# Optimization experiments

Hardware: AMD Instinct MI355X
Metric: run time of the kernel (lower is better)

## Reference

```python
import jax, jax.numpy as jnp
import numpy as np

ALPHA = 0.2  # LeakyReLU negative slope


def _gat_layer(x, W, a):
    """One GraphAttentionLayer (concat=True -> elu output).
    x: (B,N,Din); W: (Din,F); a: (2F,1).
    Faithful to source: adj mask is computed then discarded (softmax over raw e),
    so adj does not enter the math. Uses the additive decomposition
    e_ij = leakyrelu(a1.h_i + a2.h_j) which is mathematically identical to the
    dense (N,N,2F) concat in the original.
    """
    h = x @ W                      # (B,N,F)
    F = W.shape[1]
    a1, a2 = a[:F, 0], a[F:, 0]    # (F,), (F,)
    f1 = h @ a1                    # (B,N)
    f2 = h @ a2                    # (B,N)
    e = jax.nn.leaky_relu(f1[:, :, None] + f2[:, None, :], negative_slope=ALPHA)  # (B,N,N)
    att = jax.nn.softmax(e, axis=-1)
    h_prime = jnp.einsum('bnm,bmf->bnf', att, h)
    return jax.nn.elu(h_prime)


def setup_inputs() -> dict:
    key = jax.random.key(0)
    ks = jax.random.split(key, 6)
    B, N, D, H, F = 8, 1024, 256, 8, 128
    x = jax.random.normal(ks[0], (B, N, D), jnp.float32)
    adj = (jax.random.uniform(ks[1], (N, N)) > 0.9).astype(jnp.float32)
    xavier = lambda fi, fo: 1.414 * (2.0 / (fi + fo)) ** 0.5
    W_heads = jax.random.normal(ks[2], (H, D, F), jnp.float32) * xavier(D, F)
    a_heads = jax.random.normal(ks[3], (H, 2 * F, 1), jnp.float32) * xavier(2 * F, 1)
    W_out = jax.random.normal(ks[4], (H * F, F), jnp.float32) * xavier(H * F, F)
    a_out = jax.random.normal(ks[5], (2 * F, 1), jnp.float32) * xavier(2 * F, 1)
    return {"x": x, "adj": adj, "W_heads": W_heads, "a_heads": a_heads,
            "W_out": W_out, "a_out": a_out}


def reference(x, adj, W_heads, a_heads, W_out, a_out):
    # GAT.forward (dropout omitted: eval mode identity). adj unused per source bug.
    heads = jax.vmap(lambda W, a: _gat_layer(x, W, a))(W_heads, a_heads)  # (H,B,N,F)
    B, N = x.shape[0], x.shape[1]
    xc = jnp.transpose(heads, (1, 2, 0, 3)).reshape(B, N, -1)  # concat heads: (B,N,H*F)
    # out_att has concat=True (applies elu), then GAT.forward applies elu again.
    return jax.nn.elu(_gat_layer(xc, W_out, a_out))
```

## Files before the change

kernel.cpp:

```cpp
#include <hip/hip_runtime.h>
#include <math.h>

#define ALPHA 0.2f
#define LOG2E 1.44269504089f

typedef __attribute__((ext_vector_type(8))) short bf16x8;
typedef __attribute__((ext_vector_type(4))) float f32x4;

__device__ __forceinline__ float elu1(float x)  { return x > 0.f ? x : (__expf(x) - 1.f); }

__device__ __forceinline__ unsigned short f2bf(float x) {
    unsigned u = __float_as_uint(x);
    return (unsigned short)((u + 0x7fffu + ((u >> 16) & 1u)) >> 16);
}
__device__ __forceinline__ unsigned pkbf16(float a, float b) {
    return (unsigned)f2bf(a) | ((unsigned)f2bf(b) << 16);
}
__device__ __forceinline__ float bfs(unsigned short v) { return __uint_as_float((unsigned)v << 16); }
__device__ __forceinline__ unsigned pkbf_rhu(float a, float b) {
    unsigned ua = __float_as_uint(a) + 0x8000u;
    unsigned ub = __float_as_uint(b) + 0x8000u;
    return __builtin_amdgcn_perm(ub, ua, 0x07060302u);
}

__global__ __launch_bounds__(256) void cvt_w_all(
    const float* __restrict__ Wh, const float* __restrict__ Wo,
    unsigned short* __restrict__ WhT, unsigned short* __restrict__ WoT)
{
    const int z = blockIdx.z;
    const int K = (z < 8) ? 256 : 1024;
    if (blockIdx.x * 64 >= K) return;
    const float* in = (z < 8) ? (Wh + (size_t)z * K * 128) : Wo;
    unsigned short* out = (z < 8) ? (WhT + (size_t)z * 128 * K) : WoT;

    __shared__ float T[64][65];
    const int tid = threadIdx.x;
    const int k0 = blockIdx.x * 64, n0 = blockIdx.y * 64;

    const int kr = tid >> 4, nc = (tid & 15) * 4;
#pragma unroll
    for (int s = 0; s < 4; ++s) {
        float4 v = *(const float4*)(in + (size_t)(k0 + kr + s * 16) * 128 + n0 + nc);
        T[kr + s * 16][nc]     = v.x;
        T[kr + s * 16][nc + 1] = v.y;
        T[kr + s * 16][nc + 2] = v.z;
        T[kr + s * 16][nc + 3] = v.w;
    }
    __syncthreads();
    const int nr0 = tid >> 3, kc = (tid & 7) * 8;
#pragma unroll
    for (int s = 0; s < 2; ++s) {
        int nr = nr0 + s * 32;
        unsigned pk[4];
#pragma unroll
        for (int q = 0; q < 4; ++q)
            pk[q] = pkbf16(T[kc + 2 * q][nr], T[kc + 2 * q + 1][nr]);
        *(uint4*)(out + (size_t)(n0 + nr) * K + k0 + kc) = make_uint4(pk[0], pk[1], pk[2], pk[3]);
    }
}

template <int BM, int BN, int WM, int WN, int DOF, int AF32, int THREADS>
__global__ __launch_bounds__(THREADS) void gemm_t(
    const void* __restrict__ Avp, const unsigned short* __restrict__ Bt,
    unsigned short* __restrict__ Ct, int K,
    const float* __restrict__ aV, float* __restrict__ f1g, float* __restrict__ f2g)
{
    const int RM = WM / 16, RN = WN / 16;
    const int NCA = BM * 8 / THREADS, NCB = BN * 8 / THREADS;
    constexpr int SAB_A = (BM + BN) * 72;
    constexpr int SAB_B = BN * (BM + 8) + THREADS * 4;
    constexpr int SAB_SH = SAB_A > SAB_B ? SAB_A : SAB_B;
    __shared__ __align__(16) unsigned short SAB[SAB_SH];
    unsigned short (*As)[72] = (unsigned short(*)[72])SAB;
    unsigned short (*Bs)[72] = (unsigned short(*)[72])(SAB + BM * 72);
    unsigned short (*Cs)[BM + 8] = (unsigned short(*)[BM + 8])SAB;
    float* redf = (float*)(SAB + BN * (BM + 8));

    const int tid = threadIdx.x;
    const int w = tid >> 6, lane = tid & 63;
    const int n16 = lane & 15, quad = lane >> 4;
    const int WX = BM / WM;
    const int wm = (w % WX) * WM, wn = (w / WX) * WN;
    const int m0 = blockIdx.x * BM, n0 = blockIdx.y * BN;

    const float* Af = (const float*)Avp;
    const unsigned short* Ab = (const unsigned short*)Avp;
    const int ar = tid >> 2, akc = (tid & 3) * 16;

    f32x4 acc[RM][RN];
#pragma unroll
    for (int mm = 0; mm < RM; ++mm)
#pragma unroll
        for (int nn = 0; nn < RN; ++nn) acc[mm][nn] = (f32x4){0.f, 0.f, 0.f, 0.f};

    uint4 ra[NCA ? NCA : 1], rb[NCB];
    float4 raf[4];
    if (AF32) {
#pragma unroll
        for (int j = 0; j < 4; ++j)
            raf[j] = *(const float4*)(Af + (size_t)(m0 + ar) * K + akc + 4 * j);
    } else {
#pragma unroll
        for (int i = 0; i < NCA; ++i) {
            int c = tid * NCA + i, r = c >> 3, cc = (c & 7) * 8;
            ra[i] = *(const uint4*)(Ab + (size_t)(m0 + r) * K + cc);
        }
    }
#pragma unroll
    for (int i = 0; i < NCB; ++i) {
        int c = tid * NCB + i, r = c >> 3, cc = (c & 7) * 8;
        rb[i] = *(const uint4*)(Bt + (size_t)(n0 + r) * K + cc);
    }

    const int nk = K >> 6;
    for (int kt = 0; kt < nk; ++kt) {
        __syncthreads();
        if (AF32) {
            uint4 lo = make_uint4(pkbf16(raf[0].x, raf[0].y), pkbf16(raf[0].z, raf[0].w),
                                  pkbf16(raf[1].x, raf[1].y), pkbf16(raf[1].z, raf[1].w));
            uint4 hi = make_uint4(pkbf16(raf[2].x, raf[2].y), pkbf16(raf[2].z, raf[2].w),
                                  pkbf16(raf[3].x, raf[3].y), pkbf16(raf[3].z, raf[3].w));
            *(uint4*)&As[ar][akc]     = lo;
            *(uint4*)&As[ar][akc + 8] = hi;
        } else {
#pragma unroll
            for (int i = 0; i < NCA; ++i) {
                int c = tid * NCA + i, r = c >> 3, cc = (c & 7) * 8;
                *(uint4*)&As[r][cc] = ra[i];
            }
        }
#pragma unroll
        for (int i = 0; i < NCB; ++i) {
            int c = tid * NCB + i, r = c >> 3, cc = (c & 7) * 8;
            *(uint4*)&Bs[r][cc] = rb[i];
        }
        __syncthreads();
        if (kt + 1 < nk) {
            int k0 = (kt + 1) * 64;
            if (AF32) {
#pragma unroll
                for (int j = 0; j < 4; ++j)
                    raf[j] = *(const float4*)(Af + (size_t)(m0 + ar) * K + k0 + akc + 4 * j);
            } else {
#pragma unroll
                for (int i = 0; i < NCA; ++i) {
                    int c = tid * NCA + i, r = c >> 3, cc = (c & 7) * 8;
                    ra[i] = *(const uint4*)(Ab + (size_t)(m0 + r) * K + k0 + cc);
                }
            }
#pragma unroll
            for (int i = 0; i < NCB; ++i) {
                int c = tid * NCB + i, r = c >> 3, cc = (c & 7) * 8;
                rb[i] = *(const uint4*)(Bt + (size_t)(n0 + r) * K + k0 + cc);
            }
        }
#pragma unroll
        for (int ks = 0; ks < 2; ++ks) {
            bf16x8 am[RM], bn[RN];
#pragma unroll
            for (int mm = 0; mm < RM; ++mm)
                am[mm] = *(const bf16x8*)&As[wm + mm * 16 + n16][ks * 32 + quad * 8];
#pragma unroll
            for (int nn = 0; nn < RN; ++nn)
                bn[nn] = *(const bf16x8*)&Bs[wn + nn * 16 + n16][ks * 32 + quad * 8];
#pragma unroll
            for (int mm = 0; mm < RM; ++mm)
#pragma unroll
                for (int nn = 0; nn < RN; ++nn)
                    acc[mm][nn] = __builtin_amdgcn_mfma_f32_16x16x32_bf16(
                        am[mm], bn[nn], acc[mm][nn], 0, 0, 0);
        }
    }

    __syncthreads();

#pragma unroll
    for (int nn = 0; nn < RN; ++nn) {
        int n = wn + nn * 16 + n16;
#pragma unroll
        for (int mm = 0; mm < RM; ++mm) {
            int m = wm + mm * 16 + quad * 4;
            f32x4 a = acc[mm][nn];
            ushort4 o = make_ushort4(f2bf(a[0]), f2bf(a[1]), f2bf(a[2]), f2bf(a[3]));
            *(ushort4*)&Cs[n][m] = o;
        }
    }
    __syncthreads();

    const int CHUNKS = BM * 2 / 16;
    const int RPP = THREADS / CHUNKS;
    const int row = tid / CHUNKS, ch = tid % CHUNKS;
#pragma unroll
    for (int s = 0; s < BN / RPP; ++s) {
        int n = row + s * RPP;
        *(uint4*)(Ct + (size_t)(n0 + n) * 8192 + m0 + ch * 8) =
            *(const uint4*)&Cs[n][ch * 8];
    }

    if (DOF) {
        const int G = THREADS / BM;
        const int FP = 128 / G;
        const int mloc = tid % BM, fq = tid / BM;
        const float* az = aV + blockIdx.y * 256;
        float s1 = 0.f, s2 = 0.f;
#pragma unroll 8
        for (int k = 0; k < FP; ++k) {
            int f = fq * FP + k;
            float h = bfs(Cs[f][mloc]);
            s1 += h * az[f];
            s2 += h * az[128 + f];
        }
        *(float2*)&redf[(fq * BM + mloc) * 2] = make_float2(s1, s2);
        __syncthreads();
        if (tid < BM) {
            float a1 = 0.f, a2 = 0.f;
#pragma unroll
            for (int g = 0; g < G; ++g) {
                a1 += redf[(g * BM + tid) * 2];
                a2 += redf[(g * BM + tid) * 2 + 1];
            }
            f1g[(size_t)blockIdx.y * 8192 + m0 + tid] = a1;
            f2g[(size_t)blockIdx.y * 8192 + m0 + tid] = a2;
        }
    }
}

template <int NI, int NT, int THREADS>
__global__ __launch_bounds__(THREADS) void attn4(
    const unsigned short* __restrict__ hT, const float* __restrict__ f1g,
    const float* __restrict__ f2g, unsigned short* __restrict__ outb)
{
    const int N = 1024, JT = 128, JP = JT + 8;
    const int KKN = JT / 32;
    const int NW = THREADS / 64;
    const int ITILE = 16 * NI * NW;
    const int SJW = JT / 8;
    const int SR = THREADS / SJW;
    const int NTS = NT * 16 / SR;
    const int EPT = 1024 / THREADS;
    __shared__ __align__(16) unsigned short hls[2][NT * 16][JP];
    __shared__ float ul[1024], vl[1024];
    __shared__ float wred[NW];

    const int tid = threadIdx.x;
    const int w = tid >> 6, lane = tid & 63;
    const int n16 = lane & 15, quad = lane >> 4;
    const int hy = blockIdx.x;
    const int bz = blockIdx.z;
    const int ibx = blockIdx.y;
    const int hb = hy * 8 + bz;
    const int iw0 = ibx * ITILE + w * (16 * NI);

    if (EPT == 4) {
        const int j4 = tid * 4;
        float4 fv = *(const float4*)(f2g + (size_t)hb * N + j4);
        fv.x *= LOG2E; fv.y *= LOG2E; fv.z *= LOG2E; fv.w *= LOG2E;
        *(float4*)&ul[j4] = fv;
        float m4 = fmaxf(fmaxf(fv.x, fv.y), fmaxf(fv.z, fv.w));
#pragma unroll
        for (int off = 32; off; off >>= 1) m4 = fmaxf(m4, __shfl_xor(m4, off));
        if (lane == 0) wred[w] = m4;
    } else {
        const int j2 = tid * 2;
        float2 fv = *(const float2*)(f2g + (size_t)hb * N + j2);
        fv.x *= LOG2E; fv.y *= LOG2E;
        *(float2*)&ul[j2] = fv;
        float m4 = fmaxf(fv.x, fv.y);
#pragma unroll
        for (int off = 32; off; off >>= 1) m4 = fmaxf(m4, __shfl_xor(m4, off));
        if (lane == 0) wred[w] = m4;
    }

    float f1L[NI];
#pragma unroll
    for (int ii = 0; ii < NI; ++ii)
        f1L[ii] = f1g[(size_t)hb * N + iw0 + ii * 16 + n16] * LOG2E;

    const unsigned short* gsrc = hT + (size_t)(hy * 128) * 8192 + bz * 1024;
    const int sf = tid / SJW, sj = (tid % SJW) * 8;

    bf16x8 stg[NTS];
#pragma unroll
    for (int s = 0; s < NTS; ++s)
        stg[s] = *(const bf16x8*)(gsrc + (size_t)(sf + SR * s) * 8192 + sj);

    __syncthreads();
    float f2mL = wred[0];
#pragma unroll
    for (int k = 1; k < NW; ++k) f2mL = fmaxf(f2mL, wred[k]);

    if (EPT == 4) {
        const int j4 = tid * 4;
        float4 raw = *(const float4*)&ul[j4];
        float4 uu, vv;
        float d0 = raw.x - f2mL, d1 = raw.y - f2mL, d2 = raw.z - f2mL, d3 = raw.w - f2mL;
        uu.x = __builtin_amdgcn_exp2f(d0); vv.x = __builtin_amdgcn_exp2f(ALPHA * d0);
        uu.y = __builtin_amdgcn_exp2f(d1); vv.y = __builtin_amdgcn_exp2f(ALPHA * d1);
        uu.z = __builtin_amdgcn_exp2f(d2); vv.z = __builtin_amdgcn_exp2f(ALPHA * d2);
        uu.w = __builtin_amdgcn_exp2f(d3); vv.w = __builtin_amdgcn_exp2f(ALPHA * d3);
        *(float4*)&ul[j4] = uu;
        *(float4*)&vl[j4] = vv;
    } else {
        const int j2 = tid * 2;
        float2 raw = *(const float2*)&ul[j2];
        float d0 = raw.x - f2mL, d1 = raw.y - f2mL;
        float2 uu, vv;
        uu.x = __builtin_amdgcn_exp2f(d0); vv.x = __builtin_amdgcn_exp2f(ALPHA * d0);
        uu.y = __builtin_amdgcn_exp2f(d1); vv.y = __builtin_amdgcn_exp2f(ALPHA * d1);
        *(float2*)&ul[j2] = uu;
        *(float2*)&vl[j2] = vv;
    }

    float ri[NI];
#pragma unroll
    for (int ii = 0; ii < NI; ++ii)
        ri[ii] = __builtin_amdgcn_exp2f((ALPHA - 1.f) * (f1L[ii] + f2mL));

    f32x4 acc[NI][NT], accl[NI];
#pragma unroll
    for (int ii = 0; ii < NI; ++ii) {
        accl[ii] = (f32x4){0.f, 0.f, 0.f, 0.f};
#pragma unroll
        for (int t = 0; t < NT; ++t) acc[ii][t] = (f32x4){0.f, 0.f, 0.f, 0.f};
    }
    bf16x8 ones;
    { union { bf16x8 v; unsigned u[4]; } o;
      o.u[0] = o.u[1] = o.u[2] = o.u[3] = 0x3F803F80u; ones = o.v; }

#pragma unroll
    for (int s = 0; s < NTS; ++s)
        *(bf16x8*)&hls[0][sf + SR * s][sj] = stg[s];
    __syncthreads();

    for (int jt = 0; jt < N / JT; ++jt) {
        const int cur = jt & 1;
        if (jt + 1 < N / JT) {
            int j0n = (jt + 1) * JT;
#pragma unroll
            for (int s = 0; s < NTS; ++s)
                stg[s] = *(const bf16x8*)(gsrc + (size_t)(sf + SR * s) * 8192 + j0n + sj);
        }
        const int j0 = jt * JT;
#pragma unroll
        for (int kk = 0; kk < KKN; ++kk) {
            const int jb = j0 + kk * 32 + quad * 8;
            float4 u0 = *(const float4*)&ul[jb], u1 = *(const float4*)&ul[jb + 4];
            float4 v0 = *(const float4*)&vl[jb], v1 = *(const float4*)&vl[jb + 4];
            float uj[8] = {u0.x, u0.y, u0.z, u0.w, u1.x, u1.y, u1.z, u1.w};
            float vj[8] = {v0.x, v0.y, v0.z, v0.w, v1.x, v1.y, v1.z, v1.w};

            bf16x8 afr[NI];
#pragma unroll
            for (int ii = 0; ii < NI; ++ii) {
                union { bf16x8 v; unsigned u[4]; } cvt;
#pragma unroll
                for (int q = 0; q < 4; ++q) {
                    float p0 = fmaxf(uj[2 * q],     ri[ii] * vj[2 * q]);
                    float p1 = fmaxf(uj[2 * q + 1], ri[ii] * vj[2 * q + 1]);
                    cvt.u[q] = pkbf_rhu(p0, p1);
                }
                afr[ii] = cvt.v;
            }
#pragma unroll
            for (int t = 0; t < NT; ++t) {
                bf16x8 bfr = *(const bf16x8*)&hls[cur][t * 16 + n16][kk * 32 + quad * 8];
#pragma unroll
                for (int ii = 0; ii < NI; ++ii)
                    acc[ii][t] = __builtin_amdgcn_mfma_f32_16x16x32_bf16(
                        afr[ii], bfr, acc[ii][t], 0, 0, 0);
            }
#pragma unroll
            for (int ii = 0; ii < NI; ++ii)
                accl[ii] = __builtin_amdgcn_mfma_f32_16x16x32_bf16(
                    afr[ii], ones, accl[ii], 0, 0, 0);
        }
        if (jt + 1 < N / JT) {
#pragma unroll
            for (int s = 0; s < NTS; ++s)
                *(bf16x8*)&hls[1 - cur][sf + SR * s][sj] = stg[s];
        }
        __syncthreads();
    }

#pragma unroll
    for (int ii = 0; ii < NI; ++ii) {
#pragma unroll
        for (int r = 0; r < 4; ++r) {
            float inv = 1.f / accl[ii][r];
            int i = iw0 + ii * 16 + quad * 4 + r;
#pragma unroll
            for (int t = 0; t < NT; ++t) {
                float tv = acc[ii][t][r] * inv;
                tv = elu1(tv);
                outb[(size_t)(bz * 1024 + i) * 1024 + hy * 128 + t * 16 + n16] = f2bf(tv);
            }
        }
    }
}

__global__ __launch_bounds__(256) void attn5(
    const unsigned short* __restrict__ hT, const float* __restrict__ f1g,
    const float* __restrict__ f2g, float* __restrict__ outf)
{
    const int N = 1024;
    __shared__ __align__(16) unsigned short hfull[64][1032];
    __shared__ float ul[1024], vl[1024];
    __shared__ float wred[4];

    const int tid = threadIdx.x;
    const int w = tid >> 6, lane = tid & 63;
    const int n16 = lane & 15, quad = lane >> 4;
    const int bz = blockIdx.x;
    const int ibx = blockIdx.y;
    const int fz = blockIdx.z;
    const int iw0 = ibx * 64 + w * 16;

    const int j4 = tid * 4;
    {
        float4 fv = *(const float4*)(f2g + (size_t)bz * N + j4);
        fv.x *= LOG2E; fv.y *= LOG2E; fv.z *= LOG2E; fv.w *= LOG2E;
        *(float4*)&ul[j4] = fv;
        float m4 = fmaxf(fmaxf(fv.x, fv.y), fmaxf(fv.z, fv.w));
#pragma unroll
        for (int off = 32; off; off >>= 1) m4 = fmaxf(m4, __shfl_xor(m4, off));
        if (lane == 0) wred[w] = m4;
    }

    float f1L = f1g[(size_t)bz * N + iw0 + n16] * LOG2E;

    const unsigned short* gsrc = hT + (size_t)(fz * 64) * 8192 + bz * 1024;
    const int sr = tid >> 3;
    const int sc = (tid & 7) * 8;
#pragma unroll
    for (int s = 0; s < 2; ++s)
#pragma unroll
        for (int c = 0; c < 16; ++c)
            *(bf16x8*)&hfull[sr + 32 * s][sc + c * 64] =
                *(const bf16x8*)(gsrc + (size_t)(sr + 32 * s) * 8192 + sc + c * 64);

    __syncthreads();
    const float f2mL = fmaxf(fmaxf(wred[0], wred[1]), fmaxf(wred[2], wred[3]));

    {
        float4 raw = *(const float4*)&ul[j4];
        float4 uu, vv;
        float d0 = raw.x - f2mL, d1 = raw.y - f2mL, d2 = raw.z - f2mL, d3 = raw.w - f2mL;
        uu.x = __builtin_amdgcn_exp2f(d0); vv.x = __builtin_amdgcn_exp2f(ALPHA * d0);
        uu.y = __builtin_amdgcn_exp2f(d1); vv.y = __builtin_amdgcn_exp2f(ALPHA * d1);
        uu.z = __builtin_amdgcn_exp2f(d2); vv.z = __builtin_amdgcn_exp2f(ALPHA * d2);
        uu.w = __builtin_amdgcn_exp2f(d3); vv.w = __builtin_amdgcn_exp2f(ALPHA * d3);
        *(float4*)&ul[j4] = uu;
        *(float4*)&vl[j4] = vv;
    }
    const float ri = __builtin_amdgcn_exp2f((ALPHA - 1.f) * (f1L + f2mL));

    f32x4 acc[4], accl = (f32x4){0.f, 0.f, 0.f, 0.f};
#pragma unroll
    for (int t = 0; t < 4; ++t) acc[t] = (f32x4){0.f, 0.f, 0.f, 0.f};
    bf16x8 ones;
    { union { bf16x8 v; unsigned u[4]; } o;
      o.u[0] = o.u[1] = o.u[2] = o.u[3] = 0x3F803F80u; ones = o.v; }

    __syncthreads();

    for (int jt = 0; jt < 16; ++jt) {
#pragma unroll
        for (int kk = 0; kk < 2; ++kk) {
            const int jb = jt * 64 + kk * 32 + quad * 8;
            float4 u0 = *(const float4*)&ul[jb], u1 = *(const float4*)&ul[jb + 4];
            float4 v0 = *(const float4*)&vl[jb], v1 = *(const float4*)&vl[jb + 4];
            float uj[8] = {u0.x, u0.y, u0.z, u0.w, u1.x, u1.y, u1.z, u1.w};
            float vj[8] = {v0.x, v0.y, v0.z, v0.w, v1.x, v1.y, v1.z, v1.w};

            union { bf16x8 v; unsigned u[4]; } cvt;
#pragma unroll
            for (int q = 0; q < 4; ++q) {
                float p0 = fmaxf(uj[2 * q],     ri * vj[2 * q]);
                float p1 = fmaxf(uj[2 * q + 1], ri * vj[2 * q + 1]);
                cvt.u[q] = pkbf_rhu(p0, p1);
            }
            bf16x8 afr = cvt.v;
#pragma unroll
            for (int t = 0; t < 4; ++t) {
                bf16x8 bfr = *(const bf16x8*)&hfull[t * 16 + n16][jb];
                acc[t] = __builtin_amdgcn_mfma_f32_16x16x32_bf16(afr, bfr, acc[t], 0, 0, 0);
            }
            accl = __builtin_amdgcn_mfma_f32_16x16x32_bf16(afr, ones, accl, 0, 0, 0);
        }
    }

#pragma unroll
    for (int r = 0; r < 4; ++r) {
        float inv = 1.f / accl[r];
        int i = iw0 + quad * 4 + r;
#pragma unroll
        for (int t = 0; t < 4; ++t) {
            float tv = elu1(elu1(acc[t][r] * inv));
            outf[(size_t)(bz * 1024 + i) * 128 + fz * 64 + t * 16 + n16] = tv;
        }
    }
}

extern "C" void kernel_launch(void* const* d_in, const int* in_sizes, int n_in,
                              void* d_out, int out_size, void* d_ws, size_t ws_size,
                              hipStream_t stream)
{
    const float* x  = (const float*)d_in[0];
    const float* Wh = (const float*)d_in[2];
    const float* ah = (const float*)d_in[3];
    const float* Wo = (const float*)d_in[4];
    const float* ao = (const float*)d_in[5];
    float* out = (float*)d_out;

    unsigned short* WhT = (unsigned short*)d_ws;
    unsigned short* WoT = WhT + 262144;
    unsigned short* h1T = WoT + 131072;
    unsigned short* xcb = h1T + 8388608;
    unsigned short* h2T = xcb + 8388608;
    float* f1a  = (float*)(h2T + 1048576);
    float* f2a  = f1a + 65536;
    float* f1b  = f2a + 65536;
    float* f2b  = f1b + 8192;

    cvt_w_all<<<dim3(16, 2, 9), 256, 0, stream>>>(Wh, Wo, WhT, WoT);

    gemm_t<128, 128, 32, 64, 1, 1, 512><<<dim3(64, 8), 512, 0, stream>>>(
        x, WhT, h1T, 256, ah, f1a, f2a);
    attn4<2, 8, 512><<<dim3(8, 4, 8), 512, 0, stream>>>(h1T, f1a, f2a, xcb);

    gemm_t<32, 128, 16, 64, 1, 0, 256><<<dim3(256, 1), 256, 0, stream>>>(
        xcb, WoT, h2T, 1024, ao, f1b, f2b);
    attn5<<<dim3(8, 16, 2), 256, 0, stream>>>(h2T, f1b, f2b, out);
}
```

Before: 153.4 us.

## Fuse layer-2 projection GEMM and attention into one cooperative kernel with grid sync

The second-layer projection GEMM (with its f1/f2 score reductions) and the final attention kernel are merged into a single cooperative kernel of 256 blocks. A grid-wide sync separates the two phases, and both phases reuse one large shared-memory buffer. This removes a kernel launch boundary and its tail gap. In exchange it pays for the grid sync and runs both phases at the same 256-block, single-block-per-CU occupancy, since the large shared allocation likely limits residency.

```diff
diff --git a/kernel.cpp b/kernel.cpp
--- a/kernel.cpp
+++ b/kernel.cpp
@@ -1,5 +1,8 @@
 #include <hip/hip_runtime.h>
+#include <hip/hip_cooperative_groups.h>
 #include <math.h>
+
+namespace cg = cooperative_groups;
 
 #define ALPHA 0.2f
 #define LOG2E 1.44269504089f
@@ -398,105 +401,215 @@
     }
 }
 
-__global__ __launch_bounds__(256) void attn5(
-    const unsigned short* __restrict__ hT, const float* __restrict__ f1g,
-    const float* __restrict__ f2g, float* __restrict__ outf)
+__global__ __launch_bounds__(256) void l2_fused(
+    const unsigned short* __restrict__ Ab, const unsigned short* __restrict__ Bt,
+    unsigned short* __restrict__ Ct, const float* __restrict__ aV,
+    float* __restrict__ f1g, float* __restrict__ f2g, float* __restrict__ outf)
 {
-    const int N = 1024;
-    __shared__ __align__(16) unsigned short hfull[64][1032];
-    __shared__ float ul[1024], vl[1024];
-    __shared__ float wred[4];
-
+    __shared__ __align__(16) unsigned char SMEM[140320];
     const int tid = threadIdx.x;
     const int w = tid >> 6, lane = tid & 63;
     const int n16 = lane & 15, quad = lane >> 4;
-    const int bz = blockIdx.x;
-    const int ibx = blockIdx.y;
-    const int fz = blockIdx.z;
-    const int iw0 = ibx * 64 + w * 16;
-
-    const int j4 = tid * 4;
+
     {
-        float4 fv = *(const float4*)(f2g + (size_t)bz * N + j4);
-        fv.x *= LOG2E; fv.y *= LOG2E; fv.z *= LOG2E; fv.w *= LOG2E;
-        *(float4*)&ul[j4] = fv;
-        float m4 = fmaxf(fmaxf(fv.x, fv.y), fmaxf(fv.z, fv.w));
-#pragma unroll
-        for (int off = 32; off; off >>= 1) m4 = fmaxf(m4, __shfl_xor(m4, off));
-        if (lane == 0) wred[w] = m4;
-    }
-
-    float f1L = f1g[(size_t)bz * N + iw0 + n16] * LOG2E;
-
-    const unsigned short* gsrc = hT + (size_t)(fz * 64) * 8192 + bz * 1024;
-    const int sr = tid >> 3;
-    const int sc = (tid & 7) * 8;
-#pragma unroll
-    for (int s = 0; s < 2; ++s)
-#pragma unroll
-        for (int c = 0; c < 16; ++c)
-            *(bf16x8*)&hfull[sr + 32 * s][sc + c * 64] =
-                *(const bf16x8*)(gsrc + (size_t)(sr + 32 * s) * 8192 + sc + c * 64);
-
-    __syncthreads();
-    const float f2mL = fmaxf(fmaxf(wred[0], wred[1]), fmaxf(wred[2], wred[3]));
+        const int K = 1024;
+        unsigned short* SMs = (unsigned short*)SMEM;
+        unsigned short (*As)[72] = (unsigned short(*)[72])SMs;
+        unsigned short (*Bs)[72] = (unsigned short(*)[72])(SMs + 32 * 72);
+        unsigned short (*Cs)[40] = (unsigned short(*)[40])SMs;
+        float* redf = (float*)(SMs + 128 * 40);
+
+        const int wm = (w & 1) * 16, wn = (w >> 1) * 64;
+        const int m0 = blockIdx.x * 32;
+        const int ar_r = tid >> 3, ar_c = (tid & 7) * 8;
+
+        f32x4 acc[4];
+#pragma unroll
+        for (int nn = 0; nn < 4; ++nn) acc[nn] = (f32x4){0.f, 0.f, 0.f, 0.f};
+
+        uint4 ra, rb[4];
+        ra = *(const uint4*)(Ab + (size_t)(m0 + ar_r) * K + ar_c);
+#pragma unroll
+        for (int i = 0; i < 4; ++i) {
+            int c = tid * 4 + i, r = c >> 3, cc = (c & 7) * 8;
+            rb[i] = *(const uint4*)(Bt + (size_t)r * K + cc);
+        }
+
+        const int nk = K >> 6;
+        for (int kt = 0; kt < nk; ++kt) {
+            __syncthreads();
+            *(uint4*)&As[ar_r][ar_c] = ra;
+#pragma unroll
+            for (int i = 0; i < 4; ++i) {
+                int c = tid * 4 + i, r = c >> 3, cc = (c & 7) * 8;
+                *(uint4*)&Bs[r][cc] = rb[i];
+            }
+            __syncthreads();
+            if (kt + 1 < nk) {
+                int k0 = (kt + 1) * 64;
+                ra = *(const uint4*)(Ab + (size_t)(m0 + ar_r) * K + k0 + ar_c);
+#pragma unroll
+                for (int i = 0; i < 4; ++i) {
+                    int c = tid * 4 + i, r = c >> 3, cc = (c & 7) * 8;
+                    rb[i] = *(const uint4*)(Bt + (size_t)r * K + k0 + cc);
+                }
+            }
+#pragma unroll
+            for (int ks = 0; ks < 2; ++ks) {
+                bf16x8 am = *(const bf16x8*)&As[wm + n16][ks * 32 + quad * 8];
+                bf16x8 bn[4];
+#pragma unroll
+                for (int nn = 0; nn < 4; ++nn)
+                    bn[nn] = *(const bf16x8*)&Bs[wn + nn * 16 + n16][ks * 32 + quad * 8];
+#pragma unroll
+                for (int nn = 0; nn < 4; ++nn)
+                    acc[nn] = __builtin_amdgcn_mfma_f32_16x16x32_bf16(
+                        am, bn[nn], acc[nn], 0, 0, 0);
+            }
+        }
+
+        __syncthreads();
+#pragma unroll
+        for (int nn = 0; nn < 4; ++nn) {
+            int n = wn + nn * 16 + n16;
+            int m = wm + quad * 4;
+            f32x4 a = acc[nn];
+            ushort4 o = make_ushort4(f2bf(a[0]), f2bf(a[1]), f2bf(a[2]), f2bf(a[3]));
+            *(ushort4*)&Cs[n][m] = o;
+        }
+        __syncthreads();
+
+        {
+            const int row = tid >> 2, ch = tid & 3;
+#pragma unroll
+            for (int s = 0; s < 2; ++s) {
+                int n = row + s * 64;
+                *(uint4*)(Ct + (size_t)n * 8192 + m0 + ch * 8) =
+                    *(const uint4*)&Cs[n][ch * 8];
+            }
+        }
+
+        {
+            const int mloc = tid & 31, fq = tid >> 5;
+            float s1 = 0.f, s2 = 0.f;
+#pragma unroll 8
+            for (int k = 0; k < 16; ++k) {
+                int f = fq * 16 + k;
+                float h = bfs(Cs[f][mloc]);
+                s1 += h * aV[f];
+                s2 += h * aV[128 + f];
+            }
+            *(float2*)&redf[(fq * 32 + mloc) * 2] = make_float2(s1, s2);
+            __syncthreads();
+            if (tid < 32) {
+                float a1 = 0.f, a2 = 0.f;
+#pragma unroll
+                for (int g = 0; g < 8; ++g) {
+                    a1 += redf[(g * 32 + tid) * 2];
+                    a2 += redf[(g * 32 + tid) * 2 + 1];
+                }
+                f1g[m0 + tid] = a1;
+                f2g[m0 + tid] = a2;
+            }
+        }
+    }
+
+    cg::this_grid().sync();
 
     {
-        float4 raw = *(const float4*)&ul[j4];
-        float4 uu, vv;
-        float d0 = raw.x - f2mL, d1 = raw.y - f2mL, d2 = raw.z - f2mL, d3 = raw.w - f2mL;
-        uu.x = __builtin_amdgcn_exp2f(d0); vv.x = __builtin_amdgcn_exp2f(ALPHA * d0);
-        uu.y = __builtin_amdgcn_exp2f(d1); vv.y = __builtin_amdgcn_exp2f(ALPHA * d1);
-        uu.z = __builtin_amdgcn_exp2f(d2); vv.z = __builtin_amdgcn_exp2f(ALPHA * d2);
-        uu.w = __builtin_amdgcn_exp2f(d3); vv.w = __builtin_amdgcn_exp2f(ALPHA * d3);
-        *(float4*)&ul[j4] = uu;
-        *(float4*)&vl[j4] = vv;
-    }
-    const float ri = __builtin_amdgcn_exp2f((ALPHA - 1.f) * (f1L + f2mL));
-
-    f32x4 acc[4], accl = (f32x4){0.f, 0.f, 0.f, 0.f};
-#pragma unroll
-    for (int t = 0; t < 4; ++t) acc[t] = (f32x4){0.f, 0.f, 0.f, 0.f};
-    bf16x8 ones;
-    { union { bf16x8 v; unsigned u[4]; } o;
-      o.u[0] = o.u[1] = o.u[2] = o.u[3] = 0x3F803F80u; ones = o.v; }
-
-    __syncthreads();
-
-    for (int jt = 0; jt < 16; ++jt) {
-#pragma unroll
-        for (int kk = 0; kk < 2; ++kk) {
-            const int jb = jt * 64 + kk * 32 + quad * 8;
-            float4 u0 = *(const float4*)&ul[jb], u1 = *(const float4*)&ul[jb + 4];
-            float4 v0 = *(const float4*)&vl[jb], v1 = *(const float4*)&vl[jb + 4];
-            float uj[8] = {u0.x, u0.y, u0.z, u0.w, u1.x, u1.y, u1.z, u1.w};
-            float vj[8] = {v0.x, v0.y, v0.z, v0.w, v1.x, v1.y, v1.z, v1.w};
-
-            union { bf16x8 v; unsigned u[4]; } cvt;
-#pragma unroll
-            for (int q = 0; q < 4; ++q) {
-                float p0 = fmaxf(uj[2 * q],     ri * vj[2 * q]);
-                float p1 = fmaxf(uj[2 * q + 1], ri * vj[2 * q + 1]);
-                cvt.u[q] = pkbf_rhu(p0, p1);
-            }
-            bf16x8 afr = cvt.v;
+        const int N = 1024;
+        unsigned short (*hfull)[1032] = (unsigned short(*)[1032])SMEM;
+        float* ul = (float*)(SMEM + 64 * 1032 * 2);
+        float* vl = ul + 1024;
+        float* wred = vl + 1024;
+
+        const int b = blockIdx.x;
+        const int bz = b & 7, ibx = (b >> 3) & 15, fz = b >> 7;
+        const int iw0 = ibx * 64 + w * 16;
+
+        const int j4 = tid * 4;
+        {
+            float4 fv = *(const float4*)(f2g + (size_t)bz * N + j4);
+            fv.x *= LOG2E; fv.y *= LOG2E; fv.z *= LOG2E; fv.w *= LOG2E;
+            *(float4*)&ul[j4] = fv;
+            float m4 = fmaxf(fmaxf(fv.x, fv.y), fmaxf(fv.z, fv.w));
+#pragma unroll
+            for (int off = 32; off; off >>= 1) m4 = fmaxf(m4, __shfl_xor(m4, off));
+            if (lane == 0) wred[w] = m4;
+        }
+
+        float f1L = f1g[(size_t)bz * N + iw0 + n16] * LOG2E;
+
+        const unsigned short* gsrc = Ct + (size_t)(fz * 64) * 8192 + bz * 1024;
+        const int sr = tid >> 3;
+        const int sc = (tid & 7) * 8;
+#pragma unroll
+        for (int s = 0; s < 2; ++s)
+#pragma unroll
+            for (int c = 0; c < 16; ++c)
+                *(bf16x8*)&hfull[sr + 32 * s][sc + c * 64] =
+                    *(const bf16x8*)(gsrc + (size_t)(sr + 32 * s) * 8192 + sc + c * 64);
+
+        __syncthreads();
+        const float f2mL = fmaxf(fmaxf(wred[0], wred[1]), fmaxf(wred[2], wred[3]));
+
+        {
+            float4 raw = *(const float4*)&ul[j4];
+            float4 uu, vv;
+            float d0 = raw.x - f2mL, d1 = raw.y - f2mL, d2 = raw.z - f2mL, d3 = raw.w - f2mL;
+            uu.x = __builtin_amdgcn_exp2f(d0); vv.x = __builtin_amdgcn_exp2f(ALPHA * d0);
+            uu.y = __builtin_amdgcn_exp2f(d1); vv.y = __builtin_amdgcn_exp2f(ALPHA * d1);
+            uu.z = __builtin_amdgcn_exp2f(d2); vv.z = __builtin_amdgcn_exp2f(ALPHA * d2);
+            uu.w = __builtin_amdgcn_exp2f(d3); vv.w = __builtin_amdgcn_exp2f(ALPHA * d3);
+            *(float4*)&ul[j4] = uu;
+            *(float4*)&vl[j4] = vv;
+        }
+        const float ri = __builtin_amdgcn_exp2f((ALPHA - 1.f) * (f1L + f2mL));
+
+        f32x4 acc[4], accl = (f32x4){0.f, 0.f, 0.f, 0.f};
+#pragma unroll
+        for (int t = 0; t < 4; ++t) acc[t] = (f32x4){0.f, 0.f, 0.f, 0.f};
+        bf16x8 ones;
+        { union { bf16x8 v; unsigned u[4]; } o;
+          o.u[0] = o.u[1] = o.u[2] = o.u[3] = 0x3F803F80u; ones = o.v; }
+
+        __syncthreads();
+
+        for (int jt = 0; jt < 16; ++jt) {
+#pragma unroll
+            for (int kk = 0; kk < 2; ++kk) {
+                const int jb = jt * 64 + kk * 32 + quad * 8;
+                float4 u0 = *(const float4*)&ul[jb], u1 = *(const float4*)&ul[jb + 4];
+                float4 v0 = *(const float4*)&vl[jb], v1 = *(const float4*)&vl[jb + 4];
+                float uj[8] = {u0.x, u0.y, u0.z, u0.w, u1.x, u1.y, u1.z, u1.w};
+                float vj[8] = {v0.x, v0.y, v0.z, v0.w, v1.x, v1.y, v1.z, v1.w};
+
+                union { bf16x8 v; unsigned u[4]; } cvt;
+#pragma unroll
+                for (int q = 0; q < 4; ++q) {
+                    float p0 = fmaxf(uj[2 * q],     ri * vj[2 * q]);
+                    float p1 = fmaxf(uj[2 * q + 1], ri * vj[2 * q + 1]);
+                    cvt.u[q] = pkbf_rhu(p0, p1);
+                }
+                bf16x8 afr = cvt.v;
+#pragma unroll
+                for (int t = 0; t < 4; ++t) {
+                    bf16x8 bfr = *(const bf16x8*)&hfull[t * 16 + n16][jb];
+                    acc[t] = __builtin_amdgcn_mfma_f32_16x16x32_bf16(afr, bfr, acc[t], 0, 0, 0);
+                }
+                accl = __builtin_amdgcn_mfma_f32_16x16x32_bf16(afr, ones, accl, 0, 0, 0);
+            }
+        }
+
+#pragma unroll
+        for (int r = 0; r < 4; ++r) {
+            float inv = 1.f / accl[r];
+            int i = iw0 + quad * 4 + r;
 #pragma unroll
             for (int t = 0; t < 4; ++t) {
-                bf16x8 bfr = *(const bf16x8*)&hfull[t * 16 + n16][jb];
-                acc[t] = __builtin_amdgcn_mfma_f32_16x16x32_bf16(afr, bfr, acc[t], 0, 0, 0);
-            }
-            accl = __builtin_amdgcn_mfma_f32_16x16x32_bf16(afr, ones, accl, 0, 0, 0);
-        }
-    }
-
-#pragma unroll
-    for (int r = 0; r < 4; ++r) {
-        float inv = 1.f / accl[r];
-        int i = iw0 + quad * 4 + r;
-#pragma unroll
-        for (int t = 0; t < 4; ++t) {
-            float tv = elu1(elu1(acc[t][r] * inv));
-            outf[(size_t)(bz * 1024 + i) * 128 + fz * 64 + t * 16 + n16] = tv;
+                float tv = elu1(elu1(acc[t][r] * inv));
+                outf[(size_t)(bz * 1024 + i) * 128 + fz * 64 + t * 16 + n16] = tv;
+            }
         }
     }
 }
@@ -528,7 +641,10 @@
         x, WhT, h1T, 256, ah, f1a, f2a);
     attn4<2, 8, 512><<<dim3(8, 4, 8), 512, 0, stream>>>(h1T, f1a, f2a, xcb);
 
-    gemm_t<32, 128, 16, 64, 1, 0, 256><<<dim3(256, 1), 256, 0, stream>>>(
-        xcb, WoT, h2T, 1024, ao, f1b, f2b);
-    attn5<<<dim3(8, 16, 2), 256, 0, stream>>>(h2T, f1b, f2b, out);
-}
+    {
+        void* args[] = { (void*)&xcb, (void*)&WoT, (void*)&h2T, (void*)&ao,
+                         (void*)&f1b, (void*)&f2b, (void*)&out };
+        hipLaunchCooperativeKernel((const void*)l2_fused, dim3(256), dim3(256),
+                                   args, 0, stream);
+    }
+}
```

Measured after the change: 211.6 us. +37.9%, slower.
